# Performance work log

Measured on AMD Instinct MI355X. Metric: run time of the kernel, lower is better.

The kernel has to match this reference:

```python
import jax, jax.numpy as jnp
import numpy as np
from jax import lax

SEQ_LEN = 15
LATENT = 16
HIDDEN = 64
OUT = 1
BATCH = 65536


def setup_inputs() -> dict:
    key = jax.random.key(0)
    ks = jax.random.split(key, 11)
    s = lambda *shape: 1.0 / np.sqrt(HIDDEN)
    def u(k, shape):
        return jax.random.uniform(k, shape, jnp.float32, -1.0 / np.sqrt(HIDDEN), 1.0 / np.sqrt(HIDDEN))
    return {
        "z": jax.random.normal(ks[0], (BATCH, LATENT), jnp.float32),
        "Wih0": u(ks[1], (4 * HIDDEN, LATENT)),
        "Whh0": u(ks[2], (4 * HIDDEN, HIDDEN)),
        "bih0": u(ks[3], (4 * HIDDEN,)),
        "bhh0": u(ks[4], (4 * HIDDEN,)),
        "Wih1": u(ks[5], (4 * HIDDEN, HIDDEN)),
        "Whh1": u(ks[6], (4 * HIDDEN, HIDDEN)),
        "bih1": u(ks[7], (4 * HIDDEN,)),
        "bhh1": u(ks[8], (4 * HIDDEN,)),
        "Wfc": u(ks[9], (OUT, HIDDEN)),
        "bfc": u(ks[10], (OUT,)),
    }


def lstm_layer(x, Wih, Whh, bih, bhh):
    # x: [B, T, D]. PyTorch gate order: i, f, g, o.
    B, T, _ = x.shape
    H = Whh.shape[1]
    # precompute input projections for all timesteps: [T, B, 4H]
    x_proj = jnp.einsum('btd,gd->tbg', x, Wih) + (bih + bhh)

    def step(carry, xp):
        h, c = carry
        gates = xp + h @ Whh.T
        i, f, g, o = jnp.split(gates, 4, axis=-1)
        i = jax.nn.sigmoid(i)
        f = jax.nn.sigmoid(f)
        g = jnp.tanh(g)
        o = jax.nn.sigmoid(o)
        c = f * c + i * g
        h = o * jnp.tanh(c)
        return (h, c), h

    h0 = jnp.zeros((B, H), x.dtype)
    _, ys = lax.scan(step, (h0, h0), x_proj)  # ys: [T, B, H]
    return jnp.swapaxes(ys, 0, 1)  # [B, T, H]


def reference(z, Wih0, Whh0, bih0, bhh0, Wih1, Whh1, bih1, bhh1, Wfc, bfc):
    # z: [B, latent] -> repeat along time: [B, T, latent]
    x = jnp.broadcast_to(z[:, None, :], (z.shape[0], SEQ_LEN, z.shape[1]))
    h1 = lstm_layer(x, Wih0, Whh0, bih0, bhh0)
    # (inter-layer dropout is inactive in eval mode)
    h2 = lstm_layer(h1, Wih1, Whh1, bih1, bhh1)
    return h2 @ Wfc.T + bfc  # [B, T, OUT]
```

## Files before the change

### kernel.cpp

```cpp
#include <hip/hip_runtime.h>

#define TSTEPS 15
#define HID    64
#define LAT    16
#define NBATCH 65536
#define LOG2E  1.44269504088896f

typedef _Float16 v8h __attribute__((ext_vector_type(8)));
typedef _Float16 v4h __attribute__((ext_vector_type(4)));
typedef _Float16 v2h __attribute__((ext_vector_type(2)));
typedef float    v4f __attribute__((ext_vector_type(4)));

__device__ __forceinline__ v8h vzero8() {
    v8h v;
#pragma unroll
    for (int i = 0; i < 8; ++i) v[i] = (_Float16)0.0f;
    return v;
}

__device__ __forceinline__ v4h pack4(float a, float b, float c, float d) {
    const v2h lo = __builtin_bit_cast(v2h, __builtin_amdgcn_cvt_pkrtz(a, b));
    const v2h hi = __builtin_bit_cast(v2h, __builtin_amdgcn_cvt_pkrtz(c, d));
    return __builtin_shufflevector(lo, hi, 0, 1, 2, 3);
}

__device__ __forceinline__ float cell_update(float ai, float af, float ag,
                                             float ao, float& cst) {
    const float ei = __builtin_amdgcn_exp2f(-ai);
    const float ef = __builtin_amdgcn_exp2f(-af);
    const float eg = __builtin_amdgcn_exp2f(-2.0f * ag);
    const float eo = __builtin_amdgcn_exp2f(-ao);
    const float ig = (1.0f - eg) *
        __builtin_amdgcn_rcpf((1.0f + ei) * (1.0f + eg));
    const float f  = __builtin_amdgcn_rcpf(1.0f + ef);
    const float cc = fmaf(f, cst, ig);
    cst = cc;
    const float ec = __builtin_amdgcn_exp2f(cc * (-2.0f * LOG2E));
    return (1.0f - ec) *
        __builtin_amdgcn_rcpf((1.0f + eo) * (1.0f + ec));
}

__global__ __launch_bounds__(1024)
__attribute__((amdgpu_waves_per_eu(4, 4)))
void lstm2_pipe4(
        const float* __restrict__ z,
        const float* __restrict__ Wih0, const float* __restrict__ Whh0,
        const float* __restrict__ bih0, const float* __restrict__ bhh0,
        const float* __restrict__ Wih1, const float* __restrict__ Whh1,
        const float* __restrict__ bih1, const float* __restrict__ bhh1,
        const float* __restrict__ Wfc,  const float* __restrict__ bfc,
        float* __restrict__ out)
{
    __shared__ __align__(16) _Float16 wf[7 * 16 * 64 * 8];
    __shared__ __align__(16) _Float16 wfcf[2 * 64 * 8];
    __shared__ __align__(16) float    bsum1[256];
    __shared__ __align__(16) _Float16 state[16][16 * 72];

    const int tid  = threadIdx.x;
    const int wave = tid >> 6;
    const int lane = tid & 63;
    const int q    = lane >> 4;
    const int c    = lane & 15;
    const int row0 = blockIdx.x * 256 + wave * 16;

#pragma unroll 2
    for (int e = tid; e < 7 * 16 * 64 * 8; e += 1024) {
        const int j  = e & 7;
        const int lm = (e >> 3) & 63;
        const int mt = (e >> 9) & 15;
        const int p  = e >> 13;
        const int g  = mt * 16 + (lm & 15);
        const int kk = (lm >> 4) * 8 + j;
        float v;
        if (p == 0)      v = (kk < LAT) ? Wih0[g * LAT + kk]
                           : (kk == LAT ? bih0[g] + bhh0[g] : 0.0f);
        else if (p == 1) v = Whh0[g * HID + kk];
        else if (p == 2) v = Whh0[g * HID + 32 + kk];
        else if (p == 3) v = Wih1[g * HID + kk];
        else if (p == 4) v = Wih1[g * HID + 32 + kk];
        else if (p == 5) v = Whh1[g * HID + kk];
        else             v = Whh1[g * HID + 32 + kk];
        wf[e] = (_Float16)(v * LOG2E);
    }
    if (tid < 2 * 64 * 8) {
        const int e  = tid;
        const int j  = e & 7;
        const int lm = (e >> 3) & 63;
        const int kc = e >> 9;
        const int kk = kc * 32 + (lm >> 4) * 8 + j;
        wfcf[e] = ((lm & 15) == 0) ? (_Float16)Wfc[kk] : (_Float16)0.0f;
    }
    if (tid < 256) bsum1[tid] = (bih1[tid] + bhh1[tid]) * LOG2E;
    __syncthreads();

    _Float16* stW = &state[wave][0];
    const float bfcv = bfc[0];

    const v8h wfc0 = *(const v8h*)&wfcf[(0 * 64 + lane) * 8];
    const v8h wfc1 = *(const v8h*)&wfcf[(1 * 64 + lane) * 8];

    v8h zfrag = vzero8();
    if (q < 2) {
        const float* zp = z + (size_t)(row0 + c) * LAT + q * 8;
        const float4 za = *(const float4*)(zp);
        const float4 zb = *(const float4*)(zp + 4);
        zfrag[0] = (_Float16)za.x; zfrag[1] = (_Float16)za.y;
        zfrag[2] = (_Float16)za.z; zfrag[3] = (_Float16)za.w;
        zfrag[4] = (_Float16)zb.x; zfrag[5] = (_Float16)zb.y;
        zfrag[6] = (_Float16)zb.z; zfrag[7] = (_Float16)zb.w;
    }
    if (q == 2) zfrag[0] = (_Float16)1.0f;

    v8h hf0 = vzero8(), hf1 = vzero8();
    v8h gf0 = vzero8(), gf1 = vzero8();
    v4h h1pk[4];
    float c0s[16], c1s[16];
#pragma unroll
    for (int i = 0; i < 16; ++i) { c0s[i] = 0.0f; c1s[i] = 0.0f; }

#define AFRAG(pl, mt) (*(const v8h*)&wf[(((pl) * 16 + (mt)) * 64 + lane) * 8])
#define MFMA16(A, B, C) __builtin_amdgcn_mfma_f32_16x16x32_f16((A), (B), (C), 0, 0, 0)

    auto l0_part = [&]() {
#pragma unroll
        for (int a = 0; a < 4; ++a) {
            v4f acc0[4];
#pragma unroll
            for (int ty = 0; ty < 4; ++ty) {
                const int mt = 4 * ty + a;
                v4f t0 = {0.f, 0.f, 0.f, 0.f};
                t0 = MFMA16(AFRAG(0, mt), zfrag, t0);
                t0 = MFMA16(AFRAG(1, mt), hf0,   t0);
                t0 = MFMA16(AFRAG(2, mt), hf1,   t0);
                acc0[ty] = t0;
            }
            float hh[4];
#pragma unroll
            for (int r = 0; r < 4; ++r)
                hh[r] = cell_update(acc0[0][r], acc0[1][r], acc0[2][r],
                                    acc0[3][r], c0s[a * 4 + r]);
            *(v4h*)&stW[c * 72 + 16 * a + 4 * q] = pack4(hh[0], hh[1], hh[2], hh[3]);
        }
    };

    auto l1_part = [&]() {
#pragma unroll
        for (int a = 0; a < 4; ++a) {
            v4f acc1[4];
#pragma unroll
            for (int ty = 0; ty < 4; ++ty) {
                const int mt = 4 * ty + a;
                v4f t0 = *(const v4f*)&bsum1[64 * ty + 16 * a + 4 * q];
                t0 = MFMA16(AFRAG(3, mt), hf0, t0);
                t0 = MFMA16(AFRAG(4, mt), hf1, t0);
                t0 = MFMA16(AFRAG(5, mt), gf0, t0);
                t0 = MFMA16(AFRAG(6, mt), gf1, t0);
                acc1[ty] = t0;
            }
            float hh[4];
#pragma unroll
            for (int r = 0; r < 4; ++r)
                hh[r] = cell_update(acc1[0][r], acc1[1][r], acc1[2][r],
                                    acc1[3][r], c1s[a * 4 + r]);
            h1pk[a] = pack4(hh[0], hh[1], hh[2], hh[3]);
        }
    };

    auto l0_finish = [&]() {
        hf0 = *(const v8h*)&stW[c * 72 + 8 * q];
        hf1 = *(const v8h*)&stW[c * 72 + 32 + 8 * q];
    };

    auto l1_finish = [&](int trow) {
#pragma unroll
        for (int a = 0; a < 4; ++a)
            *(v4h*)&stW[c * 72 + 16 * a + 4 * q] = h1pk[a];
        gf0 = *(const v8h*)&stW[c * 72 + 8 * q];
        gf1 = *(const v8h*)&stW[c * 72 + 32 + 8 * q];
        v4f f = {0.f, 0.f, 0.f, 0.f};
        f = MFMA16(wfc0, gf0, f);
        f = MFMA16(wfc1, gf1, f);
        if (lane < 16)
            out[(size_t)(row0 + lane) * TSTEPS + trow] = f[0] + bfcv;
    };

    l0_part();
    l0_finish();

#pragma unroll 1
    for (int tt = 1; tt < TSTEPS; ++tt) {
        __asm__ __volatile__("" ::: "memory");
        l0_part();
        l1_part();
        l0_finish();
        l1_finish(tt - 1);
    }

    __asm__ __volatile__("" ::: "memory");
    l1_part();
    l1_finish(TSTEPS - 1);

#undef AFRAG
#undef MFMA16
}

extern "C" void kernel_launch(void* const* d_in, const int* in_sizes, int n_in,
                              void* d_out, int out_size, void* d_ws, size_t ws_size,
                              hipStream_t stream)
{
    (void)in_sizes; (void)n_in; (void)out_size; (void)d_ws; (void)ws_size;

    const float* z    = (const float*)d_in[0];
    const float* Wih0 = (const float*)d_in[1];
    const float* Whh0 = (const float*)d_in[2];
    const float* bih0 = (const float*)d_in[3];
    const float* bhh0 = (const float*)d_in[4];
    const float* Wih1 = (const float*)d_in[5];
    const float* Whh1 = (const float*)d_in[6];
    const float* bih1 = (const float*)d_in[7];
    const float* bhh1 = (const float*)d_in[8];
    const float* Wfc  = (const float*)d_in[9];
    const float* bfc  = (const float*)d_in[10];

    lstm2_pipe4<<<dim3(NBATCH / 256), dim3(1024), 0, stream>>>(
        z, Wih0, Whh0, bih0, bhh0, Wih1, Whh1, bih1, bhh1, Wfc, bfc,
        (float*)d_out);
}
```

Measured before the change: 248.3 us.

## Process two 16-row batch tiles per wave to reuse LDS weight fragments

Each wave now handles 32 batch rows as two interleaved 16-row MFMA tiles. Every weight fragment loaded from LDS feeds two MFMAs, which halves LDS weight traffic per row and gives each wave two independent MFMA chains for latency hiding. To make room for the doubled accumulators, cell states and fragments, the block shrinks to 512 threads and waves per EU drop from 4 to 2. The cost is half the resident waves per CU, so less latency is hidden across waves.

```diff
diff --git a/kernel.cpp b/kernel.cpp
--- a/kernel.cpp
+++ b/kernel.cpp
@@ -40,9 +40,9 @@
         __builtin_amdgcn_rcpf((1.0f + eo) * (1.0f + ec));
 }
 
-__global__ __launch_bounds__(1024)
-__attribute__((amdgpu_waves_per_eu(4, 4)))
-void lstm2_pipe4(
+__global__ __launch_bounds__(512)
+__attribute__((amdgpu_waves_per_eu(2, 2)))
+void lstm2_pipe5(
         const float* __restrict__ z,
         const float* __restrict__ Wih0, const float* __restrict__ Whh0,
         const float* __restrict__ bih0, const float* __restrict__ bhh0,
@@ -54,17 +54,17 @@
     __shared__ __align__(16) _Float16 wf[7 * 16 * 64 * 8];
     __shared__ __align__(16) _Float16 wfcf[2 * 64 * 8];
     __shared__ __align__(16) float    bsum1[256];
-    __shared__ __align__(16) _Float16 state[16][16 * 72];
+    __shared__ __align__(16) _Float16 state[8][32 * 72];
 
     const int tid  = threadIdx.x;
     const int wave = tid >> 6;
     const int lane = tid & 63;
     const int q    = lane >> 4;
     const int c    = lane & 15;
-    const int row0 = blockIdx.x * 256 + wave * 16;
+    const int row0 = blockIdx.x * 256 + wave * 32;
 
 #pragma unroll 2
-    for (int e = tid; e < 7 * 16 * 64 * 8; e += 1024) {
+    for (int e = tid; e < 7 * 16 * 64 * 8; e += 512) {
         const int j  = e & 7;
         const int lm = (e >> 3) & 63;
         const int mt = (e >> 9) & 15;
@@ -82,8 +82,7 @@
         else             v = Whh1[g * HID + 32 + kk];
         wf[e] = (_Float16)(v * LOG2E);
     }
-    if (tid < 2 * 64 * 8) {
-        const int e  = tid;
+    for (int e = tid; e < 2 * 64 * 8; e += 512) {
         const int j  = e & 7;
         const int lm = (e >> 3) & 63;
         const int kc = e >> 9;
@@ -99,24 +98,33 @@
     const v8h wfc0 = *(const v8h*)&wfcf[(0 * 64 + lane) * 8];
     const v8h wfc1 = *(const v8h*)&wfcf[(1 * 64 + lane) * 8];
 
-    v8h zfrag = vzero8();
+    v8h zfa = vzero8(), zfb = vzero8();
     if (q < 2) {
-        const float* zp = z + (size_t)(row0 + c) * LAT + q * 8;
-        const float4 za = *(const float4*)(zp);
-        const float4 zb = *(const float4*)(zp + 4);
-        zfrag[0] = (_Float16)za.x; zfrag[1] = (_Float16)za.y;
-        zfrag[2] = (_Float16)za.z; zfrag[3] = (_Float16)za.w;
-        zfrag[4] = (_Float16)zb.x; zfrag[5] = (_Float16)zb.y;
-        zfrag[6] = (_Float16)zb.z; zfrag[7] = (_Float16)zb.w;
-    }
-    if (q == 2) zfrag[0] = (_Float16)1.0f;
-
-    v8h hf0 = vzero8(), hf1 = vzero8();
-    v8h gf0 = vzero8(), gf1 = vzero8();
-    v4h h1pk[4];
-    float c0s[16], c1s[16];
-#pragma unroll
-    for (int i = 0; i < 16; ++i) { c0s[i] = 0.0f; c1s[i] = 0.0f; }
+        const float* zpa = z + (size_t)(row0 + c) * LAT + q * 8;
+        const float4 a0 = *(const float4*)(zpa);
+        const float4 a1 = *(const float4*)(zpa + 4);
+        zfa[0] = (_Float16)a0.x; zfa[1] = (_Float16)a0.y;
+        zfa[2] = (_Float16)a0.z; zfa[3] = (_Float16)a0.w;
+        zfa[4] = (_Float16)a1.x; zfa[5] = (_Float16)a1.y;
+        zfa[6] = (_Float16)a1.z; zfa[7] = (_Float16)a1.w;
+        const float* zpb = z + (size_t)(row0 + 16 + c) * LAT + q * 8;
+        const float4 b0 = *(const float4*)(zpb);
+        const float4 b1 = *(const float4*)(zpb + 4);
+        zfb[0] = (_Float16)b0.x; zfb[1] = (_Float16)b0.y;
+        zfb[2] = (_Float16)b0.z; zfb[3] = (_Float16)b0.w;
+        zfb[4] = (_Float16)b1.x; zfb[5] = (_Float16)b1.y;
+        zfb[6] = (_Float16)b1.z; zfb[7] = (_Float16)b1.w;
+    }
+    if (q == 2) { zfa[0] = (_Float16)1.0f; zfb[0] = (_Float16)1.0f; }
+
+    v8h hf0a = vzero8(), hf1a = vzero8();
+    v8h hf0b = vzero8(), hf1b = vzero8();
+    v8h gf0a = vzero8(), gf1a = vzero8();
+    v8h gf0b = vzero8(), gf1b = vzero8();
+    v4h h1pka[4], h1pkb[4];
+    float c0s[32], c1s[32];
+#pragma unroll
+    for (int i = 0; i < 32; ++i) { c0s[i] = 0.0f; c1s[i] = 0.0f; }
 
 #define AFRAG(pl, mt) (*(const v8h*)&wf[(((pl) * 16 + (mt)) * 64 + lane) * 8])
 #define MFMA16(A, B, C) __builtin_amdgcn_mfma_f32_16x16x32_f16((A), (B), (C), 0, 0, 0)
@@ -124,64 +132,94 @@
     auto l0_part = [&]() {
 #pragma unroll
         for (int a = 0; a < 4; ++a) {
-            v4f acc0[4];
+            v4f acc0a[4], acc0b[4];
 #pragma unroll
             for (int ty = 0; ty < 4; ++ty) {
                 const int mt = 4 * ty + a;
-                v4f t0 = {0.f, 0.f, 0.f, 0.f};
-                t0 = MFMA16(AFRAG(0, mt), zfrag, t0);
-                t0 = MFMA16(AFRAG(1, mt), hf0,   t0);
-                t0 = MFMA16(AFRAG(2, mt), hf1,   t0);
-                acc0[ty] = t0;
-            }
-            float hh[4];
-#pragma unroll
-            for (int r = 0; r < 4; ++r)
-                hh[r] = cell_update(acc0[0][r], acc0[1][r], acc0[2][r],
-                                    acc0[3][r], c0s[a * 4 + r]);
-            *(v4h*)&stW[c * 72 + 16 * a + 4 * q] = pack4(hh[0], hh[1], hh[2], hh[3]);
+                const v8h A0 = AFRAG(0, mt);
+                const v8h A1 = AFRAG(1, mt);
+                const v8h A2 = AFRAG(2, mt);
+                v4f ta = {0.f, 0.f, 0.f, 0.f};
+                v4f tb = {0.f, 0.f, 0.f, 0.f};
+                ta = MFMA16(A0, zfa,  ta);  tb = MFMA16(A0, zfb,  tb);
+                ta = MFMA16(A1, hf0a, ta);  tb = MFMA16(A1, hf0b, tb);
+                ta = MFMA16(A2, hf1a, ta);  tb = MFMA16(A2, hf1b, tb);
+                acc0a[ty] = ta; acc0b[ty] = tb;
+            }
+            float ha[4], hb[4];
+#pragma unroll
+            for (int r = 0; r < 4; ++r) {
+                ha[r] = cell_update(acc0a[0][r], acc0a[1][r], acc0a[2][r],
+                                    acc0a[3][r], c0s[a * 4 + r]);
+                hb[r] = cell_update(acc0b[0][r], acc0b[1][r], acc0b[2][r],
+                                    acc0b[3][r], c0s[16 + a * 4 + r]);
+            }
+            *(v4h*)&stW[c * 72 + 16 * a + 4 * q] =
+                pack4(ha[0], ha[1], ha[2], ha[3]);
+            *(v4h*)&stW[(16 + c) * 72 + 16 * a + 4 * q] =
+                pack4(hb[0], hb[1], hb[2], hb[3]);
         }
     };
 
     auto l1_part = [&]() {
 #pragma unroll
         for (int a = 0; a < 4; ++a) {
-            v4f acc1[4];
+            v4f acc1a[4], acc1b[4];
 #pragma unroll
             for (int ty = 0; ty < 4; ++ty) {
                 const int mt = 4 * ty + a;
-                v4f t0 = *(const v4f*)&bsum1[64 * ty + 16 * a + 4 * q];
-                t0 = MFMA16(AFRAG(3, mt), hf0, t0);
-                t0 = MFMA16(AFRAG(4, mt), hf1, t0);
-                t0 = MFMA16(AFRAG(5, mt), gf0, t0);
-                t0 = MFMA16(AFRAG(6, mt), gf1, t0);
-                acc1[ty] = t0;
-            }
-            float hh[4];
-#pragma unroll
-            for (int r = 0; r < 4; ++r)
-                hh[r] = cell_update(acc1[0][r], acc1[1][r], acc1[2][r],
-                                    acc1[3][r], c1s[a * 4 + r]);
-            h1pk[a] = pack4(hh[0], hh[1], hh[2], hh[3]);
+                const v8h A3 = AFRAG(3, mt);
+                const v8h A4 = AFRAG(4, mt);
+                const v8h A5 = AFRAG(5, mt);
+                const v8h A6 = AFRAG(6, mt);
+                v4f ta = *(const v4f*)&bsum1[64 * ty + 16 * a + 4 * q];
+                v4f tb = ta;
+                ta = MFMA16(A3, hf0a, ta);  tb = MFMA16(A3, hf0b, tb);
+                ta = MFMA16(A4, hf1a, ta);  tb = MFMA16(A4, hf1b, tb);
+                ta = MFMA16(A5, gf0a, ta);  tb = MFMA16(A5, gf0b, tb);
+                ta = MFMA16(A6, gf1a, ta);  tb = MFMA16(A6, gf1b, tb);
+                acc1a[ty] = ta; acc1b[ty] = tb;
+            }
+            float ha[4], hb[4];
+#pragma unroll
+            for (int r = 0; r < 4; ++r) {
+                ha[r] = cell_update(acc1a[0][r], acc1a[1][r], acc1a[2][r],
+                                    acc1a[3][r], c1s[a * 4 + r]);
+                hb[r] = cell_update(acc1b[0][r], acc1b[1][r], acc1b[2][r],
+                                    acc1b[3][r], c1s[16 + a * 4 + r]);
+            }
+            h1pka[a] = pack4(ha[0], ha[1], ha[2], ha[3]);
+            h1pkb[a] = pack4(hb[0], hb[1], hb[2], hb[3]);
         }
     };
 
     auto l0_finish = [&]() {
-        hf0 = *(const v8h*)&stW[c * 72 + 8 * q];
-        hf1 = *(const v8h*)&stW[c * 72 + 32 + 8 * q];
+        hf0a = *(const v8h*)&stW[c * 72 + 8 * q];
+        hf1a = *(const v8h*)&stW[c * 72 + 32 + 8 * q];
+        hf0b = *(const v8h*)&stW[(16 + c) * 72 + 8 * q];
+        hf1b = *(const v8h*)&stW[(16 + c) * 72 + 32 + 8 * q];
     };
 
     auto l1_finish = [&](int trow) {
 #pragma unroll
-        for (int a = 0; a < 4; ++a)
-            *(v4h*)&stW[c * 72 + 16 * a + 4 * q] = h1pk[a];
-        gf0 = *(const v8h*)&stW[c * 72 + 8 * q];
-        gf1 = *(const v8h*)&stW[c * 72 + 32 + 8 * q];
-        v4f f = {0.f, 0.f, 0.f, 0.f};
-        f = MFMA16(wfc0, gf0, f);
-        f = MFMA16(wfc1, gf1, f);
-        if (lane < 16)
-            out[(size_t)(row0 + lane) * TSTEPS + trow] = f[0] + bfcv;
+        for (int a = 0; a < 4; ++a) {
+            *(v4h*)&stW[c * 72 + 16 * a + 4 * q] = h1pka[a];
+            *(v4h*)&stW[(16 + c) * 72 + 16 * a + 4 * q] = h1pkb[a];
+        }
+        gf0a = *(const v8h*)&stW[c * 72 + 8 * q];
+        gf1a = *(const v8h*)&stW[c * 72 + 32 + 8 * q];
+        gf0b = *(const v8h*)&stW[(16 + c) * 72 + 8 * q];
+        gf1b = *(const v8h*)&stW[(16 + c) * 72 + 32 + 8 * q];
+        v4f fa = {0.f, 0.f, 0.f, 0.f};
+        v4f fb = {0.f, 0.f, 0.f, 0.f};
+        fa = MFMA16(wfc0, gf0a, fa);
+        fa = MFMA16(wfc1, gf1a, fa);
+        fb = MFMA16(wfc0, gf0b, fb);
+        fb = MFMA16(wfc1, gf1b, fb);
+        if (lane < 16) {
+            out[(size_t)(row0 + lane) * TSTEPS + trow]      = fa[0] + bfcv;
+            out[(size_t)(row0 + 16 + lane) * TSTEPS + trow] = fb[0] + bfcv;
+        }
     };
 
     l0_part();
@@ -222,7 +260,7 @@
     const float* Wfc  = (const float*)d_in[9];
     const float* bfc  = (const float*)d_in[10];
 
-    lstm2_pipe4<<<dim3(NBATCH / 256), dim3(1024), 0, stream>>>(
+    lstm2_pipe5<<<dim3(NBATCH / 256), dim3(512), 0, stream>>>(
         z, Wih0, Whh0, bih0, bhh0, Wih1, Whh1, bih1, bhh1, Wfc, bfc,
         (float*)d_out);
 }
```

Result: no change. 251.9 us (+1.4%).
